# Performance work log

Hardware: AMD Instinct MI355X
Metric: run time of the kernel (lower is better)

## Reference

```python
import jax, jax.numpy as jnp
import numpy as np

N_NODES = 100000
N_EDGES = 1600000
IN, HID, OUT = 32, 32, 16


def setup_inputs() -> dict:
    key = jax.random.key(0)
    ks = jax.random.split(key, 8)
    return {
        "features": jax.random.normal(ks[0], (N_NODES, IN), dtype=jnp.float32),
        "src": jax.random.randint(ks[1], (N_EDGES,), 0, N_NODES, dtype=jnp.int32),
        "dst": jax.random.randint(ks[2], (N_EDGES,), 0, N_NODES, dtype=jnp.int32),
        "edge_weight": jax.random.uniform(ks[3], (N_EDGES,), dtype=jnp.float32),
        "W1": jax.random.normal(ks[4], (IN, HID), dtype=jnp.float32) * 0.1,
        "b1": jnp.zeros((HID,), dtype=jnp.float32),
        "W2": jax.random.normal(ks[5], (HID, OUT), dtype=jnp.float32) * 0.1,
        "b2": jnp.zeros((OUT,), dtype=jnp.float32),
    }


def _graph_conv(h, W, b, src, dst, edge_weight, norm_src, norm_dst, n):
    # DGL GraphConv, norm='both', with edge_weight (u_mul_e aggregation)
    h = h * norm_src[:, None]          # out-degree^-0.5 on source side
    h = h @ W                          # dense transform (tiny GEMM)
    m = h[src] * edge_weight[:, None]  # gather + edge weighting  [E, d]
    agg = jax.ops.segment_sum(m, dst, num_segments=n)  # scatter-add SpMM
    return agg * norm_dst[:, None] + b # in-degree^-0.5 + bias


def reference(features, src, dst, edge_weight, W1, b1, W2, b2):
    n = features.shape[0]
    ones_e = jnp.ones_like(edge_weight)
    deg_out = jnp.clip(jax.ops.segment_sum(ones_e, src, num_segments=n), 1.0)
    deg_in = jnp.clip(jax.ops.segment_sum(ones_e, dst, num_segments=n), 1.0)
    norm_src = deg_out ** -0.5
    norm_dst = deg_in ** -0.5
    h = _graph_conv(features, W1, b1, src, dst, edge_weight, norm_src, norm_dst, n)
    h = jax.nn.relu(h)
    # dropout is identity in eval mode
    h = _graph_conv(h, W2, b2, src, dst, edge_weight, norm_src, norm_dst, n)
    return h
```

## Files before the change

kernel.cpp:

```cpp
#include <hip/hip_runtime.h>
#include <hip/hip_fp16.h>


#define NB   391
#define CAPB 5504
#define EPB  4096

__device__ __forceinline__ long nt_load_i64(const long* p) {
    return __builtin_nontemporal_load(p);
}

__global__ void partition_kernel(const int* __restrict__ src, const int* __restrict__ dst,
                                 const float* __restrict__ ew,
                                 int* __restrict__ g_cur_d, int* __restrict__ g_cur_s,
                                 int2* __restrict__ pack_part, unsigned char* __restrict__ src_part,
                                 int m) {
    __shared__ int hist_d[NB], hist_s[NB];
    __shared__ int cur_d[NB], cur_s[NB];
    int t = threadIdx.x;
    for (int i = t; i < NB; i += 256) { hist_d[i] = 0; hist_s[i] = 0; }
    __syncthreads();
    int base_e = blockIdx.x * EPB;
    int es[16]; int ed[16]; float ewv[16];
#pragma unroll
    for (int k = 0; k < 16; k++) {
        int e = base_e + k * 256 + t;
        if (e < m) { es[k] = src[e]; ed[k] = dst[e]; ewv[k] = ew[e]; }
        else ed[k] = -1;
    }
#pragma unroll
    for (int k = 0; k < 16; k++) {
        if (ed[k] >= 0) {
            atomicAdd(&hist_d[ed[k] >> 8], 1);
            atomicAdd(&hist_s[es[k] >> 8], 1);
        }
    }
    __syncthreads();
    for (int i = t; i < NB; i += 256) {
        int c = hist_d[i];
        cur_d[i] = i * CAPB + (c ? atomicAdd(&g_cur_d[i], c) : 0);
        c = hist_s[i];
        cur_s[i] = i * CAPB + (c ? atomicAdd(&g_cur_s[i], c) : 0);
    }
    __syncthreads();
#pragma unroll
    for (int k = 0; k < 16; k++) {
        if (ed[k] >= 0) {
            int d = ed[k];
            int pos = atomicAdd(&cur_d[d >> 8], 1);
            pack_part[pos] = make_int2(es[k] | ((d & 255) << 20), __float_as_int(ewv[k]));
            int ps = atomicAdd(&cur_s[es[k] >> 8], 1);
            src_part[ps] = (unsigned char)(es[k] & 255);
        }
    }
}

__global__ void csr_kernel(const int2* __restrict__ pack_part,
                           const unsigned char* __restrict__ src_part,
                           const int* __restrict__ g_cur_d, const int* __restrict__ g_cur_s,
                           int2* __restrict__ csr, int2* __restrict__ rs_cnt,
                           float* __restrict__ norm_src, float* __restrict__ norm_dst, int n) {
    __shared__ int cnt[256];
    __shared__ int rowx[256];
    __shared__ int cur[256];
    __shared__ int cnt_s[256];
    extern __shared__ int2 stage[];
    int t = threadIdx.x, b = blockIdx.x;
    if (t < 256) { cnt[t] = 0; cur[t] = 0; cnt_s[t] = 0; }
    __syncthreads();
    int count = g_cur_d[b]; if (count > CAPB) count = CAPB;
    int count_s = g_cur_s[b]; if (count_s > CAPB) count_s = CAPB;
    const int2* p = pack_part + (size_t)b * CAPB;
    const unsigned char* sp = src_part + (size_t)b * CAPB;
    for (int e = t; e < count; e += 512) atomicAdd(&cnt[p[e].x >> 20], 1);
    for (int e = t; e < count_s; e += 512) atomicAdd(&cnt_s[sp[e]], 1);
    __syncthreads();
    if (t < 256) {
        int node = b * 256 + t;
        if (node < n) {
            int cs = cnt_s[t];
            norm_src[node] = rsqrtf((float)(cs > 1 ? cs : 1));
        }
    }
    int c0 = 0;
    if (t < 256) { c0 = cnt[t]; rowx[t] = c0; }
    __syncthreads();
    for (int off = 1; off < 256; off <<= 1) {
        int v = 0;
        if (t < 256 && t >= off) v = rowx[t - off];
        __syncthreads();
        if (t < 256) rowx[t] += v;
        __syncthreads();
    }
    if (t < 256) {
        int excl = rowx[t] - c0;
        rowx[t] = excl;
        int node = b * 256 + t;
        if (node < n) {
            rs_cnt[node] = make_int2(b * CAPB + excl, c0);
            norm_dst[node] = rsqrtf((float)(c0 > 1 ? c0 : 1));
        }
    }
    __syncthreads();
    for (int e = t; e < count; e += 512) {
        int2 v = p[e];
        int dl = v.x >> 20;
        int r = atomicAdd(&cur[dl], 1);
        stage[rowx[dl] + r] = make_int2(v.x & 0x1FFFF, v.y);
    }
    __syncthreads();
    int2* outp = csr + (size_t)b * CAPB;
    for (int e = t; e < count; e += 512) outp[e] = stage[e];
}

__global__ void transform1_kernel(const float* __restrict__ feat,
                                  const float* __restrict__ norm_src,
                                  const float* __restrict__ W1,
                                  __half* __restrict__ h1, int n) {
    __shared__ float sW[32 * 32];
    __shared__ float sF[8][32];
    int t = threadIdx.x;
    for (int i = t; i < 32 * 32; i += 256) sW[i] = W1[i];
    int node0 = blockIdx.x * 8;
    int local = t >> 5, col = t & 31;
    int node = node0 + local;
    float f = 0.0f;
    if (node < n) f = feat[node * 32 + col] * norm_src[node];
    sF[local][col] = f;
    __syncthreads();
    if (node < n) {
        float acc = 0.0f;
#pragma unroll
        for (int k = 0; k < 32; k++) acc += sF[local][k] * sW[k * 32 + col];
        h1[(size_t)node * 32 + col] = __float2half(acc);
    }
}

__global__ void gather1_fused_kernel(const __half* __restrict__ h1, const int2* __restrict__ csr,
                                     const int2* __restrict__ rs_cnt,
                                     const float* __restrict__ norm_src, const float* __restrict__ norm_dst,
                                     const float* __restrict__ W2, const float* __restrict__ b1,
                                     __half* __restrict__ h2, int n) {
    __shared__ float sW2[32 * 16];
    __shared__ float sX[4][4][32];
    int t = threadIdx.x;
    for (int i = t; i < 512; i += 256) sW2[i] = W2[i];
    __syncthreads();
    int w = t >> 6, lane = t & 63;
    int q = lane >> 4;
    int dh = lane & 15;
    int node = (blockIdx.x * 4 + w) * 4 + q;
    bool valid = node < n;
    int2 rc = valid ? rs_cnt[node] : make_int2(0, 0);
    long base = rc.x;
    int c = rc.y;
    const __half2* tv = (const __half2*)h1;
    const long* csrl = (const long*)csr;
    float ax0 = 0.f, ay0 = 0.f, ax1 = 0.f, ay1 = 0.f;
    float ax2 = 0.f, ay2 = 0.f, ax3 = 0.f, ay3 = 0.f;
    int j = 0;
    for (; j + 3 < c; j += 4) {
        long q0 = nt_load_i64(csrl + base + j);
        long q1 = nt_load_i64(csrl + base + j + 1);
        long q2 = nt_load_i64(csrl + base + j + 2);
        long q3 = nt_load_i64(csrl + base + j + 3);
        float2 v0 = __half22float2(tv[(size_t)(int)q0 * 16 + dh]);
        float2 v1 = __half22float2(tv[(size_t)(int)q1 * 16 + dh]);
        float2 v2 = __half22float2(tv[(size_t)(int)q2 * 16 + dh]);
        float2 v3 = __half22float2(tv[(size_t)(int)q3 * 16 + dh]);
        float w0 = __int_as_float((int)(q0 >> 32)), w1 = __int_as_float((int)(q1 >> 32));
        float w2 = __int_as_float((int)(q2 >> 32)), w3 = __int_as_float((int)(q3 >> 32));
        ax0 += v0.x * w0; ay0 += v0.y * w0;
        ax1 += v1.x * w1; ay1 += v1.y * w1;
        ax2 += v2.x * w2; ay2 += v2.y * w2;
        ax3 += v3.x * w3; ay3 += v3.y * w3;
    }
    for (; j < c; j++) {
        long qq = nt_load_i64(csrl + base + j);
        float2 v = __half22float2(tv[(size_t)(int)qq * 16 + dh]);
        float ww = __int_as_float((int)(qq >> 32));
        ax0 += v.x * ww; ay0 += v.y * ww;
    }
    float ax = (ax0 + ax1) + (ax2 + ax3);
    float ay = (ay0 + ay1) + (ay2 + ay3);
    if (valid) {
        float nd = norm_dst[node], ns = norm_src[node];
        sX[w][q][2 * dh]     = fmaxf(ax * nd + b1[2 * dh],     0.0f) * ns;
        sX[w][q][2 * dh + 1] = fmaxf(ay * nd + b1[2 * dh + 1], 0.0f) * ns;
    }
    if (valid) {
        float o = 0.0f;
#pragma unroll
        for (int k = 0; k < 32; k++) o += sX[w][q][k] * sW2[k * 16 + dh];
        h2[(size_t)node * 16 + dh] = __float2half(o);
    }
}

__global__ void gather2_kernel(const __half* __restrict__ h2, const int2* __restrict__ csr,
                               const int2* __restrict__ rs_cnt,
                               const float* __restrict__ norm_dst, const float* __restrict__ b2,
                               float* __restrict__ out, int n) {
    int t = threadIdx.x;
    int w = t >> 6, lane = t & 63;
    int q = lane >> 3;
    int dh = lane & 7;
    int node = (blockIdx.x * 4 + w) * 8 + q;
    bool valid = node < n;
    int2 rc = valid ? rs_cnt[node] : make_int2(0, 0);
    long base = rc.x;
    int c = rc.y;
    const __half2* tv = (const __half2*)h2;
    const long* csrl = (const long*)csr;
    float ax0 = 0.f, ay0 = 0.f, ax1 = 0.f, ay1 = 0.f;
    float ax2 = 0.f, ay2 = 0.f, ax3 = 0.f, ay3 = 0.f;
    int j = 0;
    for (; j + 3 < c; j += 4) {
        long q0 = nt_load_i64(csrl + base + j);
        long q1 = nt_load_i64(csrl + base + j + 1);
        long q2 = nt_load_i64(csrl + base + j + 2);
        long q3 = nt_load_i64(csrl + base + j + 3);
        float2 v0 = __half22float2(tv[(size_t)(int)q0 * 8 + dh]);
        float2 v1 = __half22float2(tv[(size_t)(int)q1 * 8 + dh]);
        float2 v2 = __half22float2(tv[(size_t)(int)q2 * 8 + dh]);
        float2 v3 = __half22float2(tv[(size_t)(int)q3 * 8 + dh]);
        float w0 = __int_as_float((int)(q0 >> 32)), w1 = __int_as_float((int)(q1 >> 32));
        float w2 = __int_as_float((int)(q2 >> 32)), w3 = __int_as_float((int)(q3 >> 32));
        ax0 += v0.x * w0; ay0 += v0.y * w0;
        ax1 += v1.x * w1; ay1 += v1.y * w1;
        ax2 += v2.x * w2; ay2 += v2.y * w2;
        ax3 += v3.x * w3; ay3 += v3.y * w3;
    }
    for (; j < c; j++) {
        long qq = nt_load_i64(csrl + base + j);
        float2 v = __half22float2(tv[(size_t)(int)qq * 8 + dh]);
        float ww = __int_as_float((int)(qq >> 32));
        ax0 += v.x * ww; ay0 += v.y * ww;
    }
    float ax = (ax0 + ax1) + (ax2 + ax3);
    float ay = (ay0 + ay1) + (ay2 + ay3);
    if (valid) {
        float nd = norm_dst[node];
        float2 o;
        o.x = ax * nd + b2[2 * dh];
        o.y = ay * nd + b2[2 * dh + 1];
        ((float2*)out)[(size_t)node * 8 + dh] = o;
    }
}

extern "C" void kernel_launch(void* const* d_in, const int* in_sizes, int n_in,
                              void* d_out, int out_size, void* d_ws, size_t ws_size,
                              hipStream_t stream) {
    const float* feat = (const float*)d_in[0];
    const int*   src  = (const int*)d_in[1];
    const int*   dst  = (const int*)d_in[2];
    const float* ew   = (const float*)d_in[3];
    const float* W1   = (const float*)d_in[4];
    const float* b1   = (const float*)d_in[5];
    const float* W2   = (const float*)d_in[6];
    const float* b2   = (const float*)d_in[7];
    float* out = (float*)d_out;

    const int n = in_sizes[0] / 32;
    const int m = in_sizes[1];

    char* wsb = (char*)d_ws;
    int2*   pack_part = (int2*)wsb;
    int2*   csr       = pack_part + (size_t)NB * CAPB;
    __half* h1        = (__half*)(csr + (size_t)NB * CAPB);
    __half* h2        = h1 + 32 * (size_t)n;
    float*  norm_src  = (float*)(h2 + 16 * (size_t)n);
    float*  norm_dst  = norm_src + n;
    int2*   rs_cnt    = (int2*)(norm_dst + n);
    int*    g_cur_d   = (int*)(rs_cnt + n);
    int*    g_cur_s   = g_cur_d + NB;
    unsigned char* src_part = (unsigned char*)(g_cur_s + NB);

    hipMemsetAsync(g_cur_d, 0, 2 * NB * sizeof(int), stream);

    partition_kernel<<<(m + EPB - 1) / EPB, 256, 0, stream>>>(src, dst, ew, g_cur_d, g_cur_s,
                                                              pack_part, src_part, m);
    csr_kernel<<<NB, 512, CAPB * sizeof(int2), stream>>>(pack_part, src_part, g_cur_d, g_cur_s,
                                                         csr, rs_cnt, norm_src, norm_dst, n);
    transform1_kernel<<<(n + 7) / 8, 256, 0, stream>>>(feat, norm_src, W1, h1, n);
    gather1_fused_kernel<<<(n + 15) / 16, 256, 0, stream>>>(h1, csr, rs_cnt,
                                                            norm_src, norm_dst, W2, b1, h2, n);
    gather2_kernel<<<(n + 31) / 32, 256, 0, stream>>>(h2, csr, rs_cnt, norm_dst, b2, out, n);
}
```

Baseline: 213.2 us.

## Stage partitioned edges in LDS by bucket before coalesced global scatter

The partition kernel now does a local exclusive scan of the per-bucket histograms and sorts each block's edges by bucket in shared memory. It then writes them to global memory in bucket order, so consecutive threads write consecutive addresses within a bucket's segment. This targets the uncoalesced scattered 8-byte and 1-byte writes of the previous direct-atomic placement. In exchange it uses roughly 60KB of LDS per block, which limits occupancy, and adds two serial scans with many barriers.

```diff
diff --git a/kernel.cpp b/kernel.cpp
--- a/kernel.cpp
+++ b/kernel.cpp
@@ -10,22 +10,32 @@
     return __builtin_nontemporal_load(p);
 }
 
-__global__ void partition_kernel(const int* __restrict__ src, const int* __restrict__ dst,
-                                 const float* __restrict__ ew,
-                                 int* __restrict__ g_cur_d, int* __restrict__ g_cur_s,
-                                 int2* __restrict__ pack_part, unsigned char* __restrict__ src_part,
-                                 int m) {
+__global__ __launch_bounds__(256) void partition_kernel(
+        const int* __restrict__ src, const int* __restrict__ dst,
+        const float* __restrict__ ew,
+        int* __restrict__ g_cur_d, int* __restrict__ g_cur_s,
+        int2* __restrict__ pack_part, unsigned char* __restrict__ src_part, int m) {
     __shared__ int hist_d[NB], hist_s[NB];
+    __shared__ int lbase_d[NB], lbase_s[NB];
+    __shared__ int gbase_d[NB], gbase_s[NB];
     __shared__ int cur_d[NB], cur_s[NB];
+    __shared__ int sc[2][512];
+    __shared__ long stage[EPB];
+    __shared__ unsigned short dbuck[EPB];
+    __shared__ unsigned char  sstage[EPB];
+    __shared__ unsigned short sbuck[EPB];
     int t = threadIdx.x;
-    for (int i = t; i < NB; i += 256) { hist_d[i] = 0; hist_s[i] = 0; }
+    for (int i = t; i < NB; i += 256) {
+        hist_d[i] = 0; hist_s[i] = 0; cur_d[i] = 0; cur_s[i] = 0;
+    }
     __syncthreads();
     int base_e = blockIdx.x * EPB;
-    int es[16]; int ed[16]; float ewv[16];
+    int total = m - base_e; if (total > EPB) total = EPB;
+    int es[16], ed[16]; float wv[16];
 #pragma unroll
     for (int k = 0; k < 16; k++) {
         int e = base_e + k * 256 + t;
-        if (e < m) { es[k] = src[e]; ed[k] = dst[e]; ewv[k] = ew[e]; }
+        if (e < m) { es[k] = src[e]; ed[k] = dst[e]; wv[k] = ew[e]; }
         else ed[k] = -1;
     }
 #pragma unroll
@@ -36,22 +46,61 @@
         }
     }
     __syncthreads();
+    for (int i = t; i < 512; i += 256) sc[0][i] = (i < NB) ? hist_d[i] : 0;
+    __syncthreads();
+    int pp = 0;
+    for (int off = 1; off < 512; off <<= 1) {
+        for (int i = t; i < 512; i += 256)
+            sc[1 - pp][i] = sc[pp][i] + (i >= off ? sc[pp][i - off] : 0);
+        __syncthreads();
+        pp ^= 1;
+    }
+    for (int i = t; i < NB; i += 256) lbase_d[i] = sc[pp][i] - hist_d[i];
+    __syncthreads();
+    for (int i = t; i < 512; i += 256) sc[0][i] = (i < NB) ? hist_s[i] : 0;
+    __syncthreads();
+    pp = 0;
+    for (int off = 1; off < 512; off <<= 1) {
+        for (int i = t; i < 512; i += 256)
+            sc[1 - pp][i] = sc[pp][i] + (i >= off ? sc[pp][i - off] : 0);
+        __syncthreads();
+        pp ^= 1;
+    }
+    for (int i = t; i < NB; i += 256) lbase_s[i] = sc[pp][i] - hist_s[i];
+    __syncthreads();
     for (int i = t; i < NB; i += 256) {
         int c = hist_d[i];
-        cur_d[i] = i * CAPB + (c ? atomicAdd(&g_cur_d[i], c) : 0);
+        gbase_d[i] = i * CAPB + (c ? atomicAdd(&g_cur_d[i], c) : 0);
         c = hist_s[i];
-        cur_s[i] = i * CAPB + (c ? atomicAdd(&g_cur_s[i], c) : 0);
+        gbase_s[i] = i * CAPB + (c ? atomicAdd(&g_cur_s[i], c) : 0);
     }
     __syncthreads();
 #pragma unroll
     for (int k = 0; k < 16; k++) {
         if (ed[k] >= 0) {
-            int d = ed[k];
-            int pos = atomicAdd(&cur_d[d >> 8], 1);
-            pack_part[pos] = make_int2(es[k] | ((d & 255) << 20), __float_as_int(ewv[k]));
-            int ps = atomicAdd(&cur_s[es[k] >> 8], 1);
-            src_part[ps] = (unsigned char)(es[k] & 255);
+            int d = ed[k], s = es[k];
+            int bd = d >> 8;
+            int r = atomicAdd(&cur_d[bd], 1);
+            int pos = lbase_d[bd] + r;
+            stage[pos] = (long)(unsigned int)(s | ((d & 255) << 20)) |
+                         ((long)__float_as_int(wv[k]) << 32);
+            dbuck[pos] = (unsigned short)bd;
+            int bs = s >> 8;
+            int rs = atomicAdd(&cur_s[bs], 1);
+            int ps = lbase_s[bs] + rs;
+            sstage[ps] = (unsigned char)(s & 255);
+            sbuck[ps] = (unsigned short)bs;
         }
+    }
+    __syncthreads();
+    long* packl = (long*)pack_part;
+    for (int i = t; i < total; i += 256) {
+        int b = dbuck[i];
+        packl[(size_t)gbase_d[b] + (i - lbase_d[b])] = stage[i];
+    }
+    for (int i = t; i < total; i += 256) {
+        int b = sbuck[i];
+        src_part[(size_t)gbase_s[b] + (i - lbase_s[b])] = sstage[i];
     }
 }
 
```

Result: faster. 208.9 us (-2.0%).
